# Optimization experiments

Measured on AMD Instinct MI355X. Metric: run time of the kernel, lower is better.

## Reference

```python
import jax, jax.numpy as jnp
import numpy as np

QUERY_DIM = 512
KV_DIM = 64
N_AUX = 8
B = 65536
EPS = 1e-5


def setup_inputs() -> dict:
    key = jax.random.key(0)
    k1, k2, k3, k4, k5 = jax.random.split(key, 5)
    query = jax.random.normal(k1, (B, QUERY_DIM), dtype=jnp.float32)
    kv_stack = jax.random.normal(k2, (B, N_AUX, KV_DIM), dtype=jnp.float32)
    # Linear weights (torch nn.Linear stores W as [out, in]; y = x @ W.T)
    w_q = jax.random.normal(k3, (KV_DIM, QUERY_DIM), dtype=jnp.float32) / np.sqrt(QUERY_DIM)
    w_k = jax.random.normal(k4, (KV_DIM, KV_DIM), dtype=jnp.float32) / np.sqrt(KV_DIM)
    w_v = jax.random.normal(k5, (KV_DIM, KV_DIM), dtype=jnp.float32) / np.sqrt(KV_DIM)
    ln_gamma = jnp.ones((KV_DIM,), dtype=jnp.float32)
    ln_beta = jnp.zeros((KV_DIM,), dtype=jnp.float32)
    return {"query": query, "kv_stack": kv_stack, "w_q": w_q, "w_k": w_k,
            "w_v": w_v, "ln_gamma": ln_gamma, "ln_beta": ln_beta}


def reference(query, kv_stack, w_q, w_k, w_v, ln_gamma, ln_beta):
    scale = KV_DIM ** (-0.5)
    q = query @ w_q.T                                  # (B, kv_dim)
    k = jnp.einsum('bnd,ed->bne', kv_stack, w_k)       # (B, n_aux, kv_dim)
    v = jnp.einsum('bnd,ed->bne', kv_stack, w_v)       # (B, n_aux, kv_dim)
    scores = jnp.einsum('bd,bnd->bn', q, k) * scale    # (B, n_aux)
    attn_w = jax.nn.softmax(scores, axis=-1)
    out = jnp.einsum('bn,bnd->bd', attn_w, v)          # (B, kv_dim)
    # LayerNorm over last dim
    mu = jnp.mean(out, axis=-1, keepdims=True)
    var = jnp.var(out, axis=-1, keepdims=True)
    normed = (out - mu) / jnp.sqrt(var + EPS)
    return normed * ln_gamma + ln_beta
```

## Files before the change

kernel.cpp:

```cpp
#include <hip/hip_runtime.h>

#define QD 512
#define KD 64
#define NR 32
#define LDA 136
#define LDT 68
#define LDU 72

typedef __attribute__((ext_vector_type(8))) short short8;
typedef __attribute__((ext_vector_type(4))) float f32x4;
typedef __attribute__((ext_vector_type(4))) unsigned short u16x4;

static __device__ __forceinline__ unsigned short f2bf(float f) {
  unsigned u = __builtin_bit_cast(unsigned, f);
  u += 0x7FFFu + ((u >> 16) & 1u);
  return (unsigned short)(u >> 16);
}
static __device__ __forceinline__ float bf2f(unsigned short s) {
  return __builtin_bit_cast(float, (unsigned)s << 16);
}
static __device__ __forceinline__ short8 pack8(f32x4 a, f32x4 b) {
  short8 r;
  r[0] = (short)f2bf(a[0]); r[1] = (short)f2bf(a[1]);
  r[2] = (short)f2bf(a[2]); r[3] = (short)f2bf(a[3]);
  r[4] = (short)f2bf(b[0]); r[5] = (short)f2bf(b[1]);
  r[6] = (short)f2bf(b[2]); r[7] = (short)f2bf(b[3]);
  return r;
}

__global__ __launch_bounds__(256) void prep_kernel(
    const float* __restrict__ w_q, const float* __restrict__ w_k,
    const float* __restrict__ w_v, unsigned short* __restrict__ mt,
    unsigned short* __restrict__ wvb) {
  const int tid = (int)(blockIdx.x * 256 + threadIdx.x);
  if (tid < QD * KD) {
    const int c = tid >> 9;
    const int d = tid & 511;
    float acc = 0.f;
#pragma unroll 8
    for (int e = 0; e < 64; ++e)
      acc = fmaf(w_q[e * QD + d], w_k[e * KD + c], acc);
    mt[c * QD + d] = f2bf(acc);
  } else {
    const int i = tid - QD * KD;
    if (i < KD * KD) wvb[i] = f2bf(w_v[i]);
  }
}

__global__ __launch_bounds__(256) void fused_kernel(
    const float* __restrict__ query,
    const float* __restrict__ kv,
    const unsigned short* __restrict__ mt,
    const unsigned short* __restrict__ wvb,
    const float* __restrict__ gamma,
    const float* __restrict__ beta,
    float* __restrict__ out) {
  __shared__ char shbuf[NR * LDA * 2];
  unsigned short* lds_A = (unsigned short*)shbuf;
  float* lds_t = (float*)shbuf;
  __shared__ unsigned short lds_u[NR * LDU];

  const int tid  = (int)threadIdx.x;
  const int w    = tid >> 6;
  const int l    = tid & 63;
  const int m    = l & 15;
  const int quad = l >> 4;
  const long b0  = (long)blockIdx.x * NR;

  const unsigned short* mrow = mt + (w * 16 + m) * QD + quad * 8;
  short8 bf_cur[4], bf_nxt[4];
#pragma unroll
  for (int ks = 0; ks < 4; ++ks)
    bf_cur[ks] = *(const short8*)(mrow + ks * 32);

  f32x4 acc[2];
  acc[0] = (f32x4){0.f, 0.f, 0.f, 0.f};
  acc[1] = (f32x4){0.f, 0.f, 0.f, 0.f};

  const int srow = tid >> 3;
  const int cseg = tid & 7;
  const float* qbase = query + (b0 + srow) * QD + cseg * 16;
  unsigned short* abase = lds_A + srow * LDA + cseg * 16;

  f32x4 stg[4];
#pragma unroll
  for (int i = 0; i < 4; ++i) stg[i] = *(const f32x4*)(qbase + i * 4);

#pragma unroll
  for (int kc = 0; kc < 4; ++kc) {
#pragma unroll
    for (int i = 0; i < 4; ++i)
      *(u16x4*)(abase + i * 4) = (u16x4){f2bf(stg[i][0]), f2bf(stg[i][1]),
                                         f2bf(stg[i][2]), f2bf(stg[i][3])};
    __syncthreads();
    if (kc < 3) {
      const float* nq = qbase + (kc + 1) * 128;
#pragma unroll
      for (int i = 0; i < 4; ++i) stg[i] = *(const f32x4*)(nq + i * 4);
      const unsigned short* mn = mrow + (kc + 1) * 128;
#pragma unroll
      for (int ks = 0; ks < 4; ++ks)
        bf_nxt[ks] = *(const short8*)(mn + ks * 32);
    }
#pragma unroll
    for (int ks2 = 0; ks2 < 4; ++ks2) {
#pragma unroll
      for (int rt = 0; rt < 2; ++rt) {
        short8 af = *(const short8*)(lds_A + (rt * 16 + m) * LDA + ks2 * 32 + quad * 8);
        acc[rt] = __builtin_amdgcn_mfma_f32_16x16x32_bf16(af, bf_cur[ks2],
                                                          acc[rt], 0, 0, 0);
      }
    }
    __syncthreads();
    if (kc < 3) {
#pragma unroll
      for (int ks = 0; ks < 4; ++ks) bf_cur[ks] = bf_nxt[ks];
    }
  }

#pragma unroll
  for (int rt = 0; rt < 2; ++rt)
#pragma unroll
    for (int r2 = 0; r2 < 4; ++r2)
      lds_t[(rt * 16 + quad * 4 + r2) * LDT + w * 16 + m] = acc[rt][r2];
  __syncthreads();

  const int rl = w * 8 + (l >> 3);
  const int o8 = l & 7;
  const int db = o8 * 8;
  const long brow = b0 + rl;

  const float* tp = lds_t + rl * LDT + db;
  f32x4 tv0 = ((const f32x4*)tp)[0];
  f32x4 tv1 = ((const f32x4*)tp)[1];

  float s[8];
  short8 kvb[8];
#pragma unroll
  for (int n = 0; n < 8; ++n) {
    const float* kp = kv + (brow * 8 + n) * 64 + db;
    f32x4 k0 = ((const f32x4*)kp)[0];
    f32x4 k1 = ((const f32x4*)kp)[1];
    f32x4 d = tv0 * k0 + tv1 * k1;
    s[n] = d[0] + d[1] + d[2] + d[3];
    kvb[n] = pack8(k0, k1);
  }
#pragma unroll
  for (int n = 0; n < 8; ++n) {
    s[n] += __shfl_xor(s[n], 1, 64);
    s[n] += __shfl_xor(s[n], 2, 64);
    s[n] += __shfl_xor(s[n], 4, 64);
  }
  float mx = s[0];
#pragma unroll
  for (int n = 1; n < 8; ++n) mx = fmaxf(mx, s[n]);
  float ev[8];
  float esum = 0.f;
#pragma unroll
  for (int n = 0; n < 8; ++n) { ev[n] = __expf((s[n] - mx) * 0.125f); esum += ev[n]; }
  const float rinv = 1.0f / esum;

  f32x4 u0 = {0.f, 0.f, 0.f, 0.f}, u1 = u0;
#pragma unroll
  for (int n = 0; n < 8; ++n) {
    const float a = ev[n];
    short8 p = kvb[n];
    u0 += a * (f32x4){bf2f((unsigned short)p[0]), bf2f((unsigned short)p[1]),
                      bf2f((unsigned short)p[2]), bf2f((unsigned short)p[3])};
    u1 += a * (f32x4){bf2f((unsigned short)p[4]), bf2f((unsigned short)p[5]),
                      bf2f((unsigned short)p[6]), bf2f((unsigned short)p[7])};
  }
  u0 *= rinv; u1 *= rinv;
  *(short8*)(lds_u + rl * LDU + db) = pack8(u0, u1);
  __syncthreads();

  short8 wvf0 = *(const short8*)(wvb + (w * 16 + m) * 64 + quad * 8);
  short8 wvf1 = *(const short8*)(wvb + (w * 16 + m) * 64 + 32 + quad * 8);
  f32x4 o[2];
  o[0] = (f32x4){0.f, 0.f, 0.f, 0.f};
  o[1] = (f32x4){0.f, 0.f, 0.f, 0.f};
#pragma unroll
  for (int rt = 0; rt < 2; ++rt) {
    short8 a0 = *(const short8*)(lds_u + (rt * 16 + m) * LDU + quad * 8);
    o[rt] = __builtin_amdgcn_mfma_f32_16x16x32_bf16(a0, wvf0, o[rt], 0, 0, 0);
    short8 a1 = *(const short8*)(lds_u + (rt * 16 + m) * LDU + 32 + quad * 8);
    o[rt] = __builtin_amdgcn_mfma_f32_16x16x32_bf16(a1, wvf1, o[rt], 0, 0, 0);
  }
#pragma unroll
  for (int rt = 0; rt < 2; ++rt)
#pragma unroll
    for (int r2 = 0; r2 < 4; ++r2)
      lds_t[(rt * 16 + quad * 4 + r2) * LDT + w * 16 + m] = o[rt][r2];
  __syncthreads();

  const float* op = lds_t + rl * LDT + db;
  f32x4 x0 = ((const f32x4*)op)[0];
  f32x4 x1 = ((const f32x4*)op)[1];
  f32x4 sv = x0 + x1;
  f32x4 sq = x0 * x0 + x1 * x1;
  float s1 = sv[0] + sv[1] + sv[2] + sv[3];
  float s2 = sq[0] + sq[1] + sq[2] + sq[3];
  s1 += __shfl_xor(s1, 1, 64); s1 += __shfl_xor(s1, 2, 64); s1 += __shfl_xor(s1, 4, 64);
  s2 += __shfl_xor(s2, 1, 64); s2 += __shfl_xor(s2, 2, 64); s2 += __shfl_xor(s2, 4, 64);
  const float mu   = s1 * 0.015625f;
  const float var  = s2 * 0.015625f - mu * mu;
  const float rstd = rsqrtf(var + 1e-5f);
  const float* gp = gamma + db;
  const float* bp = beta + db;
  float* dst = out + brow * 64 + db;
  {
    f32x4 g0 = ((const f32x4*)gp)[0], g1 = ((const f32x4*)gp)[1];
    f32x4 e0 = ((const f32x4*)bp)[0], e1 = ((const f32x4*)bp)[1];
    ((f32x4*)dst)[0] = (x0 - mu) * rstd * g0 + e0;
    ((f32x4*)dst)[1] = (x1 - mu) * rstd * g1 + e1;
  }
}

extern "C" void kernel_launch(void* const* d_in, const int* in_sizes, int n_in,
                              void* d_out, int out_size, void* d_ws, size_t ws_size,
                              hipStream_t stream) {
  const float* query = (const float*)d_in[0];
  const float* kv    = (const float*)d_in[1];
  const float* w_q   = (const float*)d_in[2];
  const float* w_k   = (const float*)d_in[3];
  const float* w_v   = (const float*)d_in[4];
  const float* gamma = (const float*)d_in[5];
  const float* beta  = (const float*)d_in[6];
  float* out = (float*)d_out;

  unsigned short* mt  = (unsigned short*)d_ws;
  unsigned short* wvb = mt + QD * KD;

  const int Bn = in_sizes[0] / QD;

  prep_kernel<<<(QD * KD + KD * KD + 255) / 256, 256, 0, stream>>>(w_q, w_k, w_v, mt, wvb);
  fused_kernel<<<Bn / NR, 256, 0, stream>>>(query, kv, mt, wvb, gamma, beta, out);
}
```

Measured before the change: 290.8 us.

## Stage full query tile in LDS and issue kv loads up front

Loads the whole 32x512 query tile into LDS as bf16 in one pass instead of four 128-column chunks with a barrier pair each, and issues all kv_stack loads at kernel start so they overlap the query staging and GEMM. kv values are kept as packed bf16 in registers and unpacked for the score dot product, which slightly lowers precision of the scores. LDS use rises to about 33KB per block and register pressure grows from holding kv and the staged query, which may lower occupancy. The per-chunk pipelining of query loads against MFMA work is removed.

```diff
diff --git a/kernel.cpp b/kernel.cpp
--- a/kernel.cpp
+++ b/kernel.cpp
@@ -3,7 +3,7 @@
 #define QD 512
 #define KD 64
 #define NR 32
-#define LDA 136
+#define LDQ 520
 #define LDT 68
 #define LDU 72
 
@@ -55,9 +55,9 @@
     const float* __restrict__ gamma,
     const float* __restrict__ beta,
     float* __restrict__ out) {
-  __shared__ char shbuf[NR * LDA * 2];
-  unsigned short* lds_A = (unsigned short*)shbuf;
-  float* lds_t = (float*)shbuf;
+  __shared__ __align__(16) char qbuf[NR * LDQ * 2];
+  unsigned short* lds_q = (unsigned short*)qbuf;
+  float* lds_t = (float*)qbuf;
   __shared__ unsigned short lds_u[NR * LDU];
 
   const int tid  = (int)threadIdx.x;
@@ -67,6 +67,37 @@
   const int quad = l >> 4;
   const long b0  = (long)blockIdx.x * NR;
 
+  const int rl = w * 8 + (l >> 3);
+  const int o8 = l & 7;
+  const int db = o8 * 8;
+  const long brow = b0 + rl;
+
+  const float* kp = kv + brow * 512 + db;
+  f32x4 kvf[16];
+#pragma unroll
+  for (int n = 0; n < 8; ++n) {
+    kvf[2 * n]     = *(const f32x4*)(kp + n * 64);
+    kvf[2 * n + 1] = *(const f32x4*)(kp + n * 64 + 4);
+  }
+  const int srow = tid >> 3;
+  const int cseg = tid & 7;
+  const float* qsrc = query + (b0 + srow) * QD + cseg * 64;
+  unsigned short* qdst = lds_q + srow * LDQ + cseg * 64;
+#pragma unroll
+  for (int h = 0; h < 2; ++h) {
+    f32x4 qs[8];
+#pragma unroll
+    for (int i = 0; i < 8; ++i) qs[i] = *(const f32x4*)(qsrc + h * 32 + i * 4);
+#pragma unroll
+    for (int i = 0; i < 8; ++i)
+      *(u16x4*)(qdst + h * 32 + i * 4) = (u16x4){f2bf(qs[i][0]), f2bf(qs[i][1]),
+                                                 f2bf(qs[i][2]), f2bf(qs[i][3])};
+  }
+  short8 kvb[8];
+#pragma unroll
+  for (int n = 0; n < 8; ++n) kvb[n] = pack8(kvf[2 * n], kvf[2 * n + 1]);
+  __syncthreads();
+
   const unsigned short* mrow = mt + (w * 16 + m) * QD + quad * 8;
   short8 bf_cur[4], bf_nxt[4];
 #pragma unroll
@@ -77,26 +108,9 @@
   acc[0] = (f32x4){0.f, 0.f, 0.f, 0.f};
   acc[1] = (f32x4){0.f, 0.f, 0.f, 0.f};
 
-  const int srow = tid >> 3;
-  const int cseg = tid & 7;
-  const float* qbase = query + (b0 + srow) * QD + cseg * 16;
-  unsigned short* abase = lds_A + srow * LDA + cseg * 16;
-
-  f32x4 stg[4];
-#pragma unroll
-  for (int i = 0; i < 4; ++i) stg[i] = *(const f32x4*)(qbase + i * 4);
-
 #pragma unroll
   for (int kc = 0; kc < 4; ++kc) {
-#pragma unroll
-    for (int i = 0; i < 4; ++i)
-      *(u16x4*)(abase + i * 4) = (u16x4){f2bf(stg[i][0]), f2bf(stg[i][1]),
-                                         f2bf(stg[i][2]), f2bf(stg[i][3])};
-    __syncthreads();
     if (kc < 3) {
-      const float* nq = qbase + (kc + 1) * 128;
-#pragma unroll
-      for (int i = 0; i < 4; ++i) stg[i] = *(const f32x4*)(nq + i * 4);
       const unsigned short* mn = mrow + (kc + 1) * 128;
 #pragma unroll
       for (int ks = 0; ks < 4; ++ks)
@@ -104,19 +118,20 @@
     }
 #pragma unroll
     for (int ks2 = 0; ks2 < 4; ++ks2) {
+      const int kk = kc * 128 + ks2 * 32 + quad * 8;
 #pragma unroll
       for (int rt = 0; rt < 2; ++rt) {
-        short8 af = *(const short8*)(lds_A + (rt * 16 + m) * LDA + ks2 * 32 + quad * 8);
+        short8 af = *(const short8*)(lds_q + (rt * 16 + m) * LDQ + kk);
         acc[rt] = __builtin_amdgcn_mfma_f32_16x16x32_bf16(af, bf_cur[ks2],
                                                           acc[rt], 0, 0, 0);
       }
     }
-    __syncthreads();
     if (kc < 3) {
 #pragma unroll
       for (int ks = 0; ks < 4; ++ks) bf_cur[ks] = bf_nxt[ks];
     }
   }
+  __syncthreads();
 
 #pragma unroll
   for (int rt = 0; rt < 2; ++rt)
@@ -124,26 +139,21 @@
     for (int r2 = 0; r2 < 4; ++r2)
       lds_t[(rt * 16 + quad * 4 + r2) * LDT + w * 16 + m] = acc[rt][r2];
   __syncthreads();
-
-  const int rl = w * 8 + (l >> 3);
-  const int o8 = l & 7;
-  const int db = o8 * 8;
-  const long brow = b0 + rl;
 
   const float* tp = lds_t + rl * LDT + db;
   f32x4 tv0 = ((const f32x4*)tp)[0];
   f32x4 tv1 = ((const f32x4*)tp)[1];
 
   float s[8];
-  short8 kvb[8];
-#pragma unroll
-  for (int n = 0; n < 8; ++n) {
-    const float* kp = kv + (brow * 8 + n) * 64 + db;
-    f32x4 k0 = ((const f32x4*)kp)[0];
-    f32x4 k1 = ((const f32x4*)kp)[1];
+#pragma unroll
+  for (int n = 0; n < 8; ++n) {
+    short8 p = kvb[n];
+    f32x4 k0 = (f32x4){bf2f((unsigned short)p[0]), bf2f((unsigned short)p[1]),
+                       bf2f((unsigned short)p[2]), bf2f((unsigned short)p[3])};
+    f32x4 k1 = (f32x4){bf2f((unsigned short)p[4]), bf2f((unsigned short)p[5]),
+                       bf2f((unsigned short)p[6]), bf2f((unsigned short)p[7])};
     f32x4 d = tv0 * k0 + tv1 * k1;
     s[n] = d[0] + d[1] + d[2] + d[3];
-    kvb[n] = pack8(k0, k1);
   }
 #pragma unroll
   for (int n = 0; n < 8; ++n) {
@@ -160,7 +170,7 @@
   for (int n = 0; n < 8; ++n) { ev[n] = __expf((s[n] - mx) * 0.125f); esum += ev[n]; }
   const float rinv = 1.0f / esum;
 
-  f32x4 u0 = {0.f, 0.f, 0.f, 0.f}, u1 = u0;
+  f32x4 u0 = (f32x4){0.f, 0.f, 0.f, 0.f}, u1 = u0;
 #pragma unroll
   for (int n = 0; n < 8; ++n) {
     const float a = ev[n];
```

Result: slower. 299.9 us (+3.1%).
